# Optimization experiments

Measured on AMD Instinct MI355X. Metric: run time of the kernel, lower is better.

The kernel has to match this reference:

```python
import jax, jax.numpy as jnp
import numpy as np

N = 50000      # nodes
E = 800000     # edges
IN, HID, LAT = 256, 64, 32


def _gcn_conv(x, W, b, src, dst, n):
    # PyG GCNConv: out = D^{-1/2} (A + I) D^{-1/2} (X W) + b
    h = x @ W                                   # [n, out]
    ones = jnp.ones_like(src, dtype=h.dtype)
    deg = jax.ops.segment_sum(ones, dst, num_segments=n)   # includes self-loops -> deg >= 1
    dinv = jax.lax.rsqrt(deg)
    norm = dinv[src] * dinv[dst]                # [e]
    msg = h[src] * norm[:, None]                # [e, out] gather
    return jax.ops.segment_sum(msg, dst, num_segments=n) + b  # scatter-add


def setup_inputs() -> dict:
    key = jax.random.key(0)
    k1, k2, k3, k4 = jax.random.split(key, 4)
    x = jax.random.normal(k1, (N, IN), dtype=jnp.float32)
    edge_index = jax.random.randint(k2, (2, E), 0, N, dtype=jnp.int64)
    W1 = jax.random.normal(k3, (IN, HID), dtype=jnp.float32) / np.sqrt(IN)
    b1 = jnp.zeros((HID,), dtype=jnp.float32)
    W2 = jax.random.normal(k4, (HID, LAT), dtype=jnp.float32) / np.sqrt(HID)
    b2 = jnp.zeros((LAT,), dtype=jnp.float32)
    return {"x": x, "edge_index": edge_index, "W1": W1, "b1": b1, "W2": W2, "b2": b2}


def reference(x, edge_index, W1, b1, W2, b2):
    n = x.shape[0]
    loop = jnp.arange(n, dtype=edge_index.dtype)
    src = jnp.concatenate([edge_index[0], loop])   # add self-loops
    dst = jnp.concatenate([edge_index[1], loop])
    h = _gcn_conv(x, W1, b1, src, dst, n)
    h = jax.nn.relu(h)
    # F.dropout is identity in eval mode
    out = _gcn_conv(h, W2, b2, src, dst, n)
    return out
```

## Files before the change

### kernel.cpp

```cpp
#include <hip/hip_runtime.h>

#define NN 50000
#define NE 800000
#define FIN 256
#define FH 64
#define FL 32
#define DMAX 48
#define NB 196
#define NCHUNK 256
#define CHUNK 3125

typedef _Float16 half8 __attribute__((ext_vector_type(8)));
typedef _Float16 half4 __attribute__((ext_vector_type(4)));
typedef float f32x4 __attribute__((ext_vector_type(4)));

__global__ __launch_bounds__(256) void k_histA(const int* __restrict__ dst,
                                               int* __restrict__ histG,
                                               const float* __restrict__ W1,
                                               _Float16* __restrict__ wt_g) {
    __shared__ int hist[NB];
    int tid = threadIdx.x, c = blockIdx.x;
    if (tid < 64) {
        int i = c * 64 + tid;
        wt_g[(i & 63) * FIN + (i >> 6)] = (_Float16)W1[i];
    }
    for (int i = tid; i < NB; i += 256) hist[i] = 0;
    __syncthreads();
    int base = c * CHUNK;
    for (int i = tid; i < CHUNK; i += 256)
        atomicAdd(&hist[dst[base + i] >> 8], 1);
    __syncthreads();
    for (int i = tid; i < NB; i += 256) histG[i * NCHUNK + c] = hist[i];
}

__global__ __launch_bounds__(256) void k_scanA(int* __restrict__ histG,
                                               int* __restrict__ bucketTotal) {
    __shared__ int tmp[256];
    int tid = threadIdx.x, b = blockIdx.x;
    int v = histG[b * NCHUNK + tid];
    tmp[tid] = v;
    __syncthreads();
    for (int off = 1; off < 256; off <<= 1) {
        int t = (tid >= off) ? tmp[tid - off] : 0;
        __syncthreads();
        tmp[tid] += t;
        __syncthreads();
    }
    histG[b * NCHUNK + tid] = tmp[tid] - v;
    if (tid == 255) bucketTotal[b] = tmp[255];
}

__device__ __forceinline__ void scan196(const int* __restrict__ bucketTotal,
                                        int* __restrict__ tmp) {
    int tid = threadIdx.x;
    int v = (tid < NB) ? bucketTotal[tid] : 0;
    tmp[tid] = v;
    __syncthreads();
    for (int off = 1; off < 256; off <<= 1) {
        int t = (tid >= off) ? tmp[tid - off] : 0;
        __syncthreads();
        tmp[tid] += t;
        __syncthreads();
    }
}

__global__ __launch_bounds__(256) void k_scatC(const int* __restrict__ src,
                                               const int* __restrict__ dst,
                                               const int* __restrict__ histG,
                                               const int* __restrict__ bucketTotal,
                                               unsigned* __restrict__ edgesB) {
    __shared__ int tmp[256];
    __shared__ int cur[NB];
    int tid = threadIdx.x, c = blockIdx.x;
    scan196(bucketTotal, tmp);
    if (tid < NB)
        cur[tid] = ((tid == 0) ? 0 : tmp[tid - 1]) + histG[tid * NCHUNK + c];
    __syncthreads();
    int base = c * CHUNK;
    for (int i = tid; i < CHUNK; i += 256) {
        int e = base + i;
        int d = dst[e];
        int pos = atomicAdd(&cur[d >> 8], 1);
        edgesB[pos] = (unsigned)(((d & 255) << 16) | src[e]);
    }
}

__global__ __launch_bounds__(256) void k_finalD(const unsigned* __restrict__ edgesB,
                                                const int* __restrict__ bucketTotal,
                                                unsigned short* __restrict__ csr16,
                                                int* __restrict__ ideg,
                                                float* __restrict__ dinv) {
    __shared__ int tmp[256];
    __shared__ int histF[256];
    __shared__ int curF[256];
    int tid = threadIdx.x, b = blockIdx.x;
    scan196(bucketTotal, tmp);
    int lo = (b == 0) ? 0 : tmp[b - 1];
    int hi = tmp[b];
    histF[tid] = 0;
    curF[tid] = 0;
    __syncthreads();
    for (int i = lo + tid; i < hi; i += 256)
        atomicAdd(&histF[(edgesB[i] >> 16) & 255], 1);
    __syncthreads();
    int d = b * 256 + tid;
    if (d < NN) {
        int cnt = histF[tid];
        ideg[d] = min(cnt, DMAX);
        dinv[d] = rsqrtf((float)(cnt + 1));
    }
    __syncthreads();
    for (int i = lo + tid; i < hi; i += 256) {
        unsigned p = edgesB[i];
        int dl = (p >> 16) & 255;
        int k = atomicAdd(&curF[dl], 1);
        if (k < DMAX)
            csr16[(size_t)(b * 256 + dl) * DMAX + k] = (unsigned short)(p & 0xFFFF);
    }
}

#define KP 128
#define XS_LD 136

__global__ __launch_bounds__(256) void k_gemm1(const float* __restrict__ x,
                                               const _Float16* __restrict__ wt_g,
                                               const float* __restrict__ dinv,
                                               _Float16* __restrict__ h1f) {
    __shared__ _Float16 xs[64 * XS_LD];
    __shared__ _Float16 wt[64 * XS_LD];
    int nb = blockIdx.x * 64;
    int tid = threadIdx.x;
    int w = tid >> 6, l = tid & 63;
    int r16 = l & 15, g = l >> 4;

    f32x4 acc[4] = {{0.f,0.f,0.f,0.f},{0.f,0.f,0.f,0.f},{0.f,0.f,0.f,0.f},{0.f,0.f,0.f,0.f}};

    #pragma unroll
    for (int p = 0; p < 2; ++p) {
        int k0 = p * KP;
        __syncthreads();
        for (int i = tid; i < 64 * 32; i += 256) {
            int r = i >> 5, c = (i & 31) * 4;
            float4 v = make_float4(0.f, 0.f, 0.f, 0.f);
            if (nb + r < NN) v = *(const float4*)&x[(size_t)(nb + r) * FIN + k0 + c];
            half4 h; h[0] = (_Float16)v.x; h[1] = (_Float16)v.y;
                     h[2] = (_Float16)v.z; h[3] = (_Float16)v.w;
            *(half4*)&xs[r * XS_LD + c] = h;
        }
        for (int i = tid; i < 64 * 16; i += 256) {
            int r = i >> 4, c = (i & 15) * 8;
            *(half8*)&wt[r * XS_LD + c] = *(const half8*)&wt_g[r * FIN + k0 + c];
        }
        __syncthreads();
        #pragma unroll
        for (int ks = 0; ks < 4; ++ks) {
            int kk = ks * 32 + g * 8;
            half8 a = *(const half8*)&xs[(w * 16 + r16) * XS_LD + kk];
            #pragma unroll
            for (int fb = 0; fb < 4; ++fb) {
                half8 b = *(const half8*)&wt[(fb * 16 + r16) * XS_LD + kk];
                acc[fb] = __builtin_amdgcn_mfma_f32_16x16x32_f16(a, b, acc[fb], 0, 0, 0);
            }
        }
    }
    int nodeb = nb + w * 16 + g * 4;
    #pragma unroll
    for (int r = 0; r < 4; ++r) {
        int node = nodeb + r;
        if (node < NN) {
            float di = dinv[node];
            #pragma unroll
            for (int fb = 0; fb < 4; ++fb)
                h1f[(size_t)node * FH + fb * 16 + r16] = (_Float16)(acc[fb][r] * di);
        }
    }
}

__global__ __launch_bounds__(256) void k_gather1(const _Float16* __restrict__ h1f,
                                                 const float* __restrict__ dinv,
                                                 const int* __restrict__ ideg,
                                                 const unsigned short* __restrict__ csr16,
                                                 const float* __restrict__ b1,
                                                 _Float16* __restrict__ h2) {
    int wid = blockIdx.x * 4 + (threadIdx.x >> 6);
    int lane = threadIdx.x & 63;
    int dl = lane >> 3, fg = lane & 7;
    int d = wid * 8 + dl;
    if (d >= NN) return;
    int row = d * DMAX;
    int cnt = ideg[d];
    float dd = dinv[d];
    float a[8];
    {
        half8 hv = *(const half8*)&h1f[(size_t)d * FH + fg * 8];
        #pragma unroll
        for (int k = 0; k < 8; ++k) a[k] = (float)hv[k];
    }
    int j = 0;
    for (; j + 4 <= cnt; j += 4) {
        unsigned p0 = *(const unsigned*)&csr16[row + j];
        unsigned p1 = *(const unsigned*)&csr16[row + j + 2];
        int s0 = p0 & 0xFFFF, s1 = p0 >> 16;
        int s2 = p1 & 0xFFFF, s3 = p1 >> 16;
        half8 v0 = *(const half8*)&h1f[(size_t)s0 * FH + fg * 8];
        half8 v1 = *(const half8*)&h1f[(size_t)s1 * FH + fg * 8];
        half8 v2 = *(const half8*)&h1f[(size_t)s2 * FH + fg * 8];
        half8 v3 = *(const half8*)&h1f[(size_t)s3 * FH + fg * 8];
        #pragma unroll
        for (int k = 0; k < 8; ++k)
            a[k] += ((float)v0[k] + (float)v1[k]) + ((float)v2[k] + (float)v3[k]);
    }
    for (; j < cnt; ++j) {
        int s = csr16[row + j];
        half8 hv = *(const half8*)&h1f[(size_t)s * FH + fg * 8];
        #pragma unroll
        for (int k = 0; k < 8; ++k) a[k] += (float)hv[k];
    }
    float4 bv0 = *(const float4*)&b1[fg * 8];
    float4 bv1 = *(const float4*)&b1[fg * 8 + 4];
    float bv[8] = {bv0.x, bv0.y, bv0.z, bv0.w, bv1.x, bv1.y, bv1.z, bv1.w};
    half8 r;
    #pragma unroll
    for (int k = 0; k < 8; ++k)
        r[k] = (_Float16)fmaxf(a[k] * dd + bv[k], 0.f);
    *(half8*)&h2[(size_t)d * FH + fg * 8] = r;
}

__global__ __launch_bounds__(256) void k_gemm2(const _Float16* __restrict__ h2,
                                               const float* __restrict__ W2,
                                               const float* __restrict__ dinv,
                                               _Float16* __restrict__ h3f) {
    __shared__ float xs[64 * FH];
    int nb = blockIdx.x * 64;
    for (int idx = threadIdx.x; idx < 64 * (FH / 4); idx += 256) {
        int r = idx >> 4;
        int c = (idx & 15) * 4;
        float4 v = make_float4(0.f, 0.f, 0.f, 0.f);
        if (nb + r < NN) {
            half4 hv = *(const half4*)&h2[(size_t)(nb + r) * FH + c];
            v.x = (float)hv[0]; v.y = (float)hv[1];
            v.z = (float)hv[2]; v.w = (float)hv[3];
        }
        *(float4*)&xs[r * FH + ((c + 4 * r) & (FH - 1))] = v;
    }
    __syncthreads();

    int f0 = (threadIdx.x & 7) * 4;
    int n0 = (threadIdx.x >> 3) * 2;
    const float* wp = W2 + f0;
    float4 a0 = make_float4(0.f, 0.f, 0.f, 0.f);
    float4 a1 = a0;
    #pragma unroll 4
    for (int k = 0; k < FH; k += 4) {
        float4 w0 = *(const float4*)&wp[(k + 0) * FL];
        float4 w1 = *(const float4*)&wp[(k + 1) * FL];
        float4 w2 = *(const float4*)&wp[(k + 2) * FL];
        float4 w3 = *(const float4*)&wp[(k + 3) * FL];
        float4 x0 = *(const float4*)&xs[(n0 + 0) * FH + ((k + 4 * (n0 + 0)) & (FH - 1))];
        float4 x1 = *(const float4*)&xs[(n0 + 1) * FH + ((k + 4 * (n0 + 1)) & (FH - 1))];
        a0.x += x0.x*w0.x + x0.y*w1.x + x0.z*w2.x + x0.w*w3.x;
        a0.y += x0.x*w0.y + x0.y*w1.y + x0.z*w2.y + x0.w*w3.y;
        a0.z += x0.x*w0.z + x0.y*w1.z + x0.z*w2.z + x0.w*w3.z;
        a0.w += x0.x*w0.w + x0.y*w1.w + x0.z*w2.w + x0.w*w3.w;
        a1.x += x1.x*w0.x + x1.y*w1.x + x1.z*w2.x + x1.w*w3.x;
        a1.y += x1.x*w0.y + x1.y*w1.y + x1.z*w2.y + x1.w*w3.y;
        a1.z += x1.x*w0.z + x1.y*w1.z + x1.z*w2.z + x1.w*w3.z;
        a1.w += x1.x*w0.w + x1.y*w1.w + x1.z*w2.w + x1.w*w3.w;
    }
    int g0 = nb + n0;
    if (g0 + 0 < NN) {
        float di = dinv[g0 + 0];
        half4 h; h[0]=(_Float16)(a0.x*di); h[1]=(_Float16)(a0.y*di);
                 h[2]=(_Float16)(a0.z*di); h[3]=(_Float16)(a0.w*di);
        *(half4*)&h3f[(size_t)(g0 + 0) * FL + f0] = h;
    }
    if (g0 + 1 < NN) {
        float di = dinv[g0 + 1];
        half4 h; h[0]=(_Float16)(a1.x*di); h[1]=(_Float16)(a1.y*di);
                 h[2]=(_Float16)(a1.z*di); h[3]=(_Float16)(a1.w*di);
        *(half4*)&h3f[(size_t)(g0 + 1) * FL + f0] = h;
    }
}

__global__ __launch_bounds__(256) void k_gather2(const _Float16* __restrict__ h3f,
                                                 const float* __restrict__ dinv,
                                                 const int* __restrict__ ideg,
                                                 const unsigned short* __restrict__ csr16,
                                                 const float* __restrict__ b2,
                                                 float* __restrict__ out) {
    int wid = blockIdx.x * 4 + (threadIdx.x >> 6);
    int lane = threadIdx.x & 63;
    int dl = lane >> 2, fg = lane & 3;
    int d = wid * 16 + dl;
    if (d >= NN) return;
    int row = d * DMAX;
    int cnt = ideg[d];
    float dd = dinv[d];
    float a[8];
    {
        half8 hv = *(const half8*)&h3f[(size_t)d * FL + fg * 8];
        #pragma unroll
        for (int k = 0; k < 8; ++k) a[k] = (float)hv[k];
    }
    int j = 0;
    for (; j + 4 <= cnt; j += 4) {
        unsigned p0 = *(const unsigned*)&csr16[row + j];
        unsigned p1 = *(const unsigned*)&csr16[row + j + 2];
        int s0 = p0 & 0xFFFF, s1 = p0 >> 16;
        int s2 = p1 & 0xFFFF, s3 = p1 >> 16;
        half8 v0 = *(const half8*)&h3f[(size_t)s0 * FL + fg * 8];
        half8 v1 = *(const half8*)&h3f[(size_t)s1 * FL + fg * 8];
        half8 v2 = *(const half8*)&h3f[(size_t)s2 * FL + fg * 8];
        half8 v3 = *(const half8*)&h3f[(size_t)s3 * FL + fg * 8];
        #pragma unroll
        for (int k = 0; k < 8; ++k)
            a[k] += ((float)v0[k] + (float)v1[k]) + ((float)v2[k] + (float)v3[k]);
    }
    for (; j < cnt; ++j) {
        int s = csr16[row + j];
        half8 hv = *(const half8*)&h3f[(size_t)s * FL + fg * 8];
        #pragma unroll
        for (int k = 0; k < 8; ++k) a[k] += (float)hv[k];
    }
    float4 bv0 = *(const float4*)&b2[fg * 8];
    float4 bv1 = *(const float4*)&b2[fg * 8 + 4];
    float4 r0, r1;
    r0.x = a[0] * dd + bv0.x;
    r0.y = a[1] * dd + bv0.y;
    r0.z = a[2] * dd + bv0.z;
    r0.w = a[3] * dd + bv0.w;
    r1.x = a[4] * dd + bv1.x;
    r1.y = a[5] * dd + bv1.y;
    r1.z = a[6] * dd + bv1.z;
    r1.w = a[7] * dd + bv1.w;
    *(float4*)&out[(size_t)d * FL + fg * 8] = r0;
    *(float4*)&out[(size_t)d * FL + fg * 8 + 4] = r1;
}

extern "C" void kernel_launch(void* const* d_in, const int* in_sizes, int n_in,
                              void* d_out, int out_size, void* d_ws, size_t ws_size,
                              hipStream_t stream) {
    const float* x  = (const float*)d_in[0];
    const int*   ei = (const int*)d_in[1];
    const float* W1 = (const float*)d_in[2];
    const float* b1 = (const float*)d_in[3];
    const float* W2 = (const float*)d_in[4];
    const float* b2 = (const float*)d_in[5];
    float* out = (float*)d_out;

    const int* src = ei;
    const int* dst = ei + NE;

    char* ws = (char*)d_ws;
    float*          dinv        = (float*)(ws);
    int*            ideg        = (int*)(ws + (size_t)(256u << 10));
    _Float16*       wt_g        = (_Float16*)(ws + (size_t)(512u << 10));
    int*            bucketTotal = (int*)(ws + (size_t)(544u << 10));
    int*            histG       = (int*)(ws + (size_t)(552u << 10));
    unsigned*       edgesB      = (unsigned*)(ws + (size_t)(768u << 10));
    unsigned short* csr16       = (unsigned short*)(ws + (size_t)(4u << 20));
    _Float16*       h1f         = (_Float16*)(ws + (size_t)(9u << 20));
    _Float16*       h2          = (_Float16*)(ws + (size_t)(16u << 20));
    _Float16*       h3f         = h1f;

    hipLaunchKernelGGL(k_histA, dim3(NCHUNK), dim3(256), 0, stream, dst, histG, W1, wt_g);
    hipLaunchKernelGGL(k_scanA, dim3(NB), dim3(256), 0, stream, histG, bucketTotal);
    hipLaunchKernelGGL(k_scatC, dim3(NCHUNK), dim3(256), 0, stream,
                       src, dst, histG, bucketTotal, edgesB);
    hipLaunchKernelGGL(k_finalD, dim3(NB), dim3(256), 0, stream,
                       edgesB, bucketTotal, csr16, ideg, dinv);

    hipLaunchKernelGGL(k_gemm1, dim3((NN + 63) / 64), dim3(256), 0, stream, x, wt_g, dinv, h1f);
    hipLaunchKernelGGL(k_gather1, dim3((NN + 31) / 32), dim3(256), 0, stream,
                       h1f, dinv, ideg, csr16, b1, h2);

    hipLaunchKernelGGL(k_gemm2, dim3((NN + 63) / 64), dim3(256), 0, stream, h2, W2, dinv, h3f);
    hipLaunchKernelGGL(k_gather2, dim3((NN + 63) / 64), dim3(256), 0, stream,
                       h3f, dinv, ideg, csr16, b2, out);
}
```

Measured before the change: 94.24 us.

## Fuse layer-2 GEMM into layer-1 gather epilogue via shared memory

The layer-1 aggregation kernel now keeps its 32 ReLU'd output rows in shared memory and multiplies them by W2, which is staged in LDS, writing the normalized h3f directly. This drops the separate k_gemm2 launch along with the h2 write and re-read through global memory. h3f moves to its own buffer because h1f is still being read by other blocks while the fused kernel writes. In exchange each block adds a W2 load (8 KB), extra LDS use and a __syncthreads, which may reduce occupancy of the gather kernel.

```diff
diff --git a/kernel.cpp b/kernel.cpp
--- a/kernel.cpp
+++ b/kernel.cpp
@@ -181,104 +181,89 @@
                                                  const int* __restrict__ ideg,
                                                  const unsigned short* __restrict__ csr16,
                                                  const float* __restrict__ b1,
-                                                 _Float16* __restrict__ h2) {
-    int wid = blockIdx.x * 4 + (threadIdx.x >> 6);
-    int lane = threadIdx.x & 63;
+                                                 const float* __restrict__ W2,
+                                                 _Float16* __restrict__ h3f) {
+    __shared__ float h2s[32][68];
+    __shared__ float w2s[FH * FL];
+    __shared__ float dds[32];
+    int tid = threadIdx.x;
+    for (int i = tid; i < FH * FL / 4; i += 256)
+        *(float4*)&w2s[i * 4] = *(const float4*)&W2[i * 4];
+
+    int base_d = blockIdx.x * 32;
+    int lane = tid & 63;
     int dl = lane >> 3, fg = lane & 7;
-    int d = wid * 8 + dl;
-    if (d >= NN) return;
-    int row = d * DMAX;
-    int cnt = ideg[d];
-    float dd = dinv[d];
-    float a[8];
-    {
-        half8 hv = *(const half8*)&h1f[(size_t)d * FH + fg * 8];
-        #pragma unroll
-        for (int k = 0; k < 8; ++k) a[k] = (float)hv[k];
-    }
-    int j = 0;
-    for (; j + 4 <= cnt; j += 4) {
-        unsigned p0 = *(const unsigned*)&csr16[row + j];
-        unsigned p1 = *(const unsigned*)&csr16[row + j + 2];
-        int s0 = p0 & 0xFFFF, s1 = p0 >> 16;
-        int s2 = p1 & 0xFFFF, s3 = p1 >> 16;
-        half8 v0 = *(const half8*)&h1f[(size_t)s0 * FH + fg * 8];
-        half8 v1 = *(const half8*)&h1f[(size_t)s1 * FH + fg * 8];
-        half8 v2 = *(const half8*)&h1f[(size_t)s2 * FH + fg * 8];
-        half8 v3 = *(const half8*)&h1f[(size_t)s3 * FH + fg * 8];
-        #pragma unroll
-        for (int k = 0; k < 8; ++k)
-            a[k] += ((float)v0[k] + (float)v1[k]) + ((float)v2[k] + (float)v3[k]);
-    }
-    for (; j < cnt; ++j) {
-        int s = csr16[row + j];
-        half8 hv = *(const half8*)&h1f[(size_t)s * FH + fg * 8];
-        #pragma unroll
-        for (int k = 0; k < 8; ++k) a[k] += (float)hv[k];
-    }
-    float4 bv0 = *(const float4*)&b1[fg * 8];
-    float4 bv1 = *(const float4*)&b1[fg * 8 + 4];
-    float bv[8] = {bv0.x, bv0.y, bv0.z, bv0.w, bv1.x, bv1.y, bv1.z, bv1.w};
-    half8 r;
-    #pragma unroll
-    for (int k = 0; k < 8; ++k)
-        r[k] = (_Float16)fmaxf(a[k] * dd + bv[k], 0.f);
-    *(half8*)&h2[(size_t)d * FH + fg * 8] = r;
-}
-
-__global__ __launch_bounds__(256) void k_gemm2(const _Float16* __restrict__ h2,
-                                               const float* __restrict__ W2,
-                                               const float* __restrict__ dinv,
-                                               _Float16* __restrict__ h3f) {
-    __shared__ float xs[64 * FH];
-    int nb = blockIdx.x * 64;
-    for (int idx = threadIdx.x; idx < 64 * (FH / 4); idx += 256) {
-        int r = idx >> 4;
-        int c = (idx & 15) * 4;
-        float4 v = make_float4(0.f, 0.f, 0.f, 0.f);
-        if (nb + r < NN) {
-            half4 hv = *(const half4*)&h2[(size_t)(nb + r) * FH + c];
-            v.x = (float)hv[0]; v.y = (float)hv[1];
-            v.z = (float)hv[2]; v.w = (float)hv[3];
-        }
-        *(float4*)&xs[r * FH + ((c + 4 * r) & (FH - 1))] = v;
-    }
-    __syncthreads();
-
-    int f0 = (threadIdx.x & 7) * 4;
-    int n0 = (threadIdx.x >> 3) * 2;
-    const float* wp = W2 + f0;
-    float4 a0 = make_float4(0.f, 0.f, 0.f, 0.f);
-    float4 a1 = a0;
-    #pragma unroll 4
-    for (int k = 0; k < FH; k += 4) {
-        float4 w0 = *(const float4*)&wp[(k + 0) * FL];
-        float4 w1 = *(const float4*)&wp[(k + 1) * FL];
-        float4 w2 = *(const float4*)&wp[(k + 2) * FL];
-        float4 w3 = *(const float4*)&wp[(k + 3) * FL];
-        float4 x0 = *(const float4*)&xs[(n0 + 0) * FH + ((k + 4 * (n0 + 0)) & (FH - 1))];
-        float4 x1 = *(const float4*)&xs[(n0 + 1) * FH + ((k + 4 * (n0 + 1)) & (FH - 1))];
-        a0.x += x0.x*w0.x + x0.y*w1.x + x0.z*w2.x + x0.w*w3.x;
-        a0.y += x0.x*w0.y + x0.y*w1.y + x0.z*w2.y + x0.w*w3.y;
-        a0.z += x0.x*w0.z + x0.y*w1.z + x0.z*w2.z + x0.w*w3.z;
-        a0.w += x0.x*w0.w + x0.y*w1.w + x0.z*w2.w + x0.w*w3.w;
-        a1.x += x1.x*w0.x + x1.y*w1.x + x1.z*w2.x + x1.w*w3.x;
-        a1.y += x1.x*w0.y + x1.y*w1.y + x1.z*w2.y + x1.w*w3.y;
-        a1.z += x1.x*w0.z + x1.y*w1.z + x1.z*w2.z + x1.w*w3.z;
-        a1.w += x1.x*w0.w + x1.y*w1.w + x1.z*w2.w + x1.w*w3.w;
-    }
-    int g0 = nb + n0;
-    if (g0 + 0 < NN) {
-        float di = dinv[g0 + 0];
-        half4 h; h[0]=(_Float16)(a0.x*di); h[1]=(_Float16)(a0.y*di);
-                 h[2]=(_Float16)(a0.z*di); h[3]=(_Float16)(a0.w*di);
-        *(half4*)&h3f[(size_t)(g0 + 0) * FL + f0] = h;
-    }
-    if (g0 + 1 < NN) {
-        float di = dinv[g0 + 1];
-        half4 h; h[0]=(_Float16)(a1.x*di); h[1]=(_Float16)(a1.y*di);
-                 h[2]=(_Float16)(a1.z*di); h[3]=(_Float16)(a1.w*di);
-        *(half4*)&h3f[(size_t)(g0 + 1) * FL + f0] = h;
+    int dlb = (tid >> 6) * 8 + dl;
+    int d = base_d + dlb;
+
+    if (d < NN) {
+        int row = d * DMAX;
+        int cnt = ideg[d];
+        float dd = dinv[d];
+        float a[8];
+        {
+            half8 hv = *(const half8*)&h1f[(size_t)d * FH + fg * 8];
+            #pragma unroll
+            for (int k = 0; k < 8; ++k) a[k] = (float)hv[k];
+        }
+        int j = 0;
+        for (; j + 4 <= cnt; j += 4) {
+            unsigned p0 = *(const unsigned*)&csr16[row + j];
+            unsigned p1 = *(const unsigned*)&csr16[row + j + 2];
+            int s0 = p0 & 0xFFFF, s1 = p0 >> 16;
+            int s2 = p1 & 0xFFFF, s3 = p1 >> 16;
+            half8 v0 = *(const half8*)&h1f[(size_t)s0 * FH + fg * 8];
+            half8 v1 = *(const half8*)&h1f[(size_t)s1 * FH + fg * 8];
+            half8 v2 = *(const half8*)&h1f[(size_t)s2 * FH + fg * 8];
+            half8 v3 = *(const half8*)&h1f[(size_t)s3 * FH + fg * 8];
+            #pragma unroll
+            for (int k = 0; k < 8; ++k)
+                a[k] += ((float)v0[k] + (float)v1[k]) + ((float)v2[k] + (float)v3[k]);
+        }
+        for (; j < cnt; ++j) {
+            int s = csr16[row + j];
+            half8 hv = *(const half8*)&h1f[(size_t)s * FH + fg * 8];
+            #pragma unroll
+            for (int k = 0; k < 8; ++k) a[k] += (float)hv[k];
+        }
+        float4 bv0 = *(const float4*)&b1[fg * 8];
+        float4 bv1 = *(const float4*)&b1[fg * 8 + 4];
+        float4 r0, r1;
+        r0.x = fmaxf(a[0] * dd + bv0.x, 0.f);
+        r0.y = fmaxf(a[1] * dd + bv0.y, 0.f);
+        r0.z = fmaxf(a[2] * dd + bv0.z, 0.f);
+        r0.w = fmaxf(a[3] * dd + bv0.w, 0.f);
+        r1.x = fmaxf(a[4] * dd + bv1.x, 0.f);
+        r1.y = fmaxf(a[5] * dd + bv1.y, 0.f);
+        r1.z = fmaxf(a[6] * dd + bv1.z, 0.f);
+        r1.w = fmaxf(a[7] * dd + bv1.w, 0.f);
+        *(float4*)&h2s[dlb][fg * 8] = r0;
+        *(float4*)&h2s[dlb][fg * 8 + 4] = r1;
+        if (fg == 0) dds[dlb] = dd;
+    }
+    __syncthreads();
+
+    int d2l = tid >> 3;
+    int d2 = base_d + d2l;
+    if (d2 < NN) {
+        int fs = (tid & 7) * 4;
+        float ddl = dds[d2l];
+        f32x4 acc = {0.f, 0.f, 0.f, 0.f};
+        #pragma unroll 8
+        for (int k = 0; k < FH; ++k) {
+            float hv = h2s[d2l][k];
+            float4 wv = *(const float4*)&w2s[k * FL + fs];
+            acc[0] += hv * wv.x;
+            acc[1] += hv * wv.y;
+            acc[2] += hv * wv.z;
+            acc[3] += hv * wv.w;
+        }
+        half4 h;
+        h[0] = (_Float16)(acc[0] * ddl);
+        h[1] = (_Float16)(acc[1] * ddl);
+        h[2] = (_Float16)(acc[2] * ddl);
+        h[3] = (_Float16)(acc[3] * ddl);
+        *(half4*)&h3f[(size_t)d2 * FL + fs] = h;
     }
 }
 
@@ -360,8 +345,8 @@
     unsigned*       edgesB      = (unsigned*)(ws + (size_t)(768u << 10));
     unsigned short* csr16       = (unsigned short*)(ws + (size_t)(4u << 20));
     _Float16*       h1f         = (_Float16*)(ws + (size_t)(9u << 20));
-    _Float16*       h2          = (_Float16*)(ws + (size_t)(16u << 20));
     _Float16*       h3f         = h1f;
+    h3f = (_Float16*)(ws + (size_t)(16u << 20));
 
     hipLaunchKernelGGL(k_histA, dim3(NCHUNK), dim3(256), 0, stream, dst, histG, W1, wt_g);
     hipLaunchKernelGGL(k_scanA, dim3(NB), dim3(256), 0, stream, histG, bucketTotal);
@@ -372,9 +357,8 @@
 
     hipLaunchKernelGGL(k_gemm1, dim3((NN + 63) / 64), dim3(256), 0, stream, x, wt_g, dinv, h1f);
     hipLaunchKernelGGL(k_gather1, dim3((NN + 31) / 32), dim3(256), 0, stream,
-                       h1f, dinv, ideg, csr16, b1, h2);
-
-    hipLaunchKernelGGL(k_gemm2, dim3((NN + 63) / 64), dim3(256), 0, stream, h2, W2, dinv, h3f);
+                       h1f, dinv, ideg, csr16, b1, W2, h3f);
+
     hipLaunchKernelGGL(k_gather2, dim3((NN + 63) / 64), dim3(256), 0, stream,
                        h3f, dinv, ideg, csr16, b2, out);
 }
```

Measured after the change: 81.86 us. 1.15x faster.
